# Kernel optimization log

Measured on AMD Instinct MI355X. Metric: run time of the kernel, lower is better.

The kernel has to match this reference:

```python
import jax, jax.numpy as jnp
import numpy as np

N_TAGS = 128
ROOT = 126
END = 127
NEG = -10000.0


def setup_inputs() -> dict:
    key = jax.random.key(0)
    k1, k2, k3, k4 = jax.random.split(key, 4)
    bsz, T = 256, 256
    feats = jax.random.normal(k1, (bsz, T, N_TAGS), jnp.float32)
    tags = jax.random.randint(k2, (bsz, T), 0, ROOT)  # never ROOT/END
    lengths = jax.random.randint(k3, (bsz,), 1, T + 1)
    mask = (jnp.arange(T)[None, :] < lengths[:, None]).astype(jnp.int32)
    # xavier_normal_: std = gain * sqrt(2 / (fan_in + fan_out))
    std = np.float32(np.sqrt(2.0 / (2 * N_TAGS)))
    lt = jax.random.normal(k4, (N_TAGS, N_TAGS), jnp.float32) * std
    lt = lt.at[:, ROOT].set(NEG).at[END, :].set(NEG)
    return {"feats": feats, "tags": tags, "mask": mask, "log_transitions": lt}


def _neg_log_likelihood(feats, log_transitions, tags, maskf):
    bsz, T, n = feats.shape
    # ---- forward belief propagation (log partition) ----
    init = log_transitions[ROOT, :] + feats[:, 0, :]  # [b, n]

    def step(fv, xs):
        feat, m = xs  # feat: [b, n], m: [b]
        # logsumexp over previous tag axis; emission is independent of it
        nxt = jax.nn.logsumexp(fv[:, :, None] + log_transitions[None, :, :], axis=1) + feat
        return jnp.where(m[:, None] > 0, nxt, fv), None

    feats_t = jnp.swapaxes(feats, 0, 1)  # [T, b, n]
    fv, _ = jax.lax.scan(step, init, (feats_t[1:], maskf[:, 1:].T))
    partition = jax.nn.logsumexp(fv + log_transitions[:, END][None, :], axis=1)  # [b]

    # ---- gold path score ----
    trans_tt = log_transitions[tags[:, :-1], tags[:, 1:]]                         # [b, T-1]
    emis = jnp.take_along_axis(feats[:, :-1, :], tags[:, :-1, None], axis=2)[..., 0]
    scores = log_transitions[ROOT, tags[:, 0]]
    scores = scores + jnp.sum(trans_tt * maskf[:, 1:] + emis * maskf[:, :-1], axis=1)
    last_idx = (maskf.sum(axis=1) - 1.0).astype(jnp.int32)                         # [b]
    last_tags = jnp.take_along_axis(tags, last_idx[:, None], axis=1)[:, 0]
    last_input = jnp.take_along_axis(feats[:, -1, :], last_tags[:, None], axis=1)[:, 0]
    scores = scores + log_transitions[last_tags, END] + last_input * maskf[:, -1]

    return jnp.mean(partition - scores)


def reference(feats, tags, mask, log_transitions):
    maskf = mask.astype(feats.dtype)
    return _neg_log_likelihood(feats, log_transitions, tags, maskf)
```

## Files before the change

kernel.cpp:

```cpp
#include <hip/hip_runtime.h>
#include <hip/hip_bf16.h>

#define N_TAGS 128
#define T_LEN  256
#define BSZ    256
#define ROOT_T 126
#define END_T  127

typedef _Float16 h2 __attribute__((ext_vector_type(2)));
typedef int   i32x4 __attribute__((ext_vector_type(4)));

static __device__ __forceinline__ h2 pkrtz(float a, float b) {
  return __builtin_bit_cast(h2, __builtin_amdgcn_cvt_pkrtz(a, b));
}
static __device__ __forceinline__ float rfl(float x) {
  return __int_as_float(__builtin_amdgcn_readfirstlane(__float_as_int(x)));
}
static __device__ __forceinline__ h2 rdl(h2 v, int k) {
  return __builtin_bit_cast(h2, __builtin_amdgcn_readlane(__builtin_bit_cast(int, v), k));
}
static __device__ __forceinline__ float fdot2(h2 a, h2 b, float c) {
#if __has_builtin(__builtin_amdgcn_fdot2)
  return __builtin_amdgcn_fdot2(a, b, c, false);
#else
  float d;
  asm("v_dot2_f32_f16 %0, %1, %2, %3" : "=v"(d) : "v"(a), "v"(b), "v"(c));
  return d;
#endif
}
static __device__ __forceinline__ float wave_max(float x) {
  #pragma unroll
  for (int d = 1; d < 64; d <<= 1) x = fmaxf(x, __shfl_xor(x, d));
  return x;
}

static __device__ __forceinline__ void dotRL(h2 vp,
                                             const h2 (&EA)[64], const h2 (&EB)[64],
                                             float& s0, float& s1) {
  float a0=0.f,a1=0.f,a2=0.f,a3=0.f, b0=0.f,b1=0.f,b2=0.f,b3=0.f;
  #pragma unroll
  for (int q = 0; q < 64; q += 4) {
    const h2 u0 = rdl(vp, q + 0);
    const h2 u1 = rdl(vp, q + 1);
    const h2 u2 = rdl(vp, q + 2);
    const h2 u3 = rdl(vp, q + 3);
    a0 = fdot2(u0, EA[q + 0], a0);  b0 = fdot2(u0, EB[q + 0], b0);
    a1 = fdot2(u1, EA[q + 1], a1);  b1 = fdot2(u1, EB[q + 1], b1);
    a2 = fdot2(u2, EA[q + 2], a2);  b2 = fdot2(u2, EB[q + 2], b2);
    a3 = fdot2(u3, EA[q + 3], a3);  b3 = fdot2(u3, EB[q + 3], b3);
  }
  s0 = (a0 + a1) + (a2 + a3);
  s1 = (b0 + b1) + (b2 + b3);
}

__global__ void
__attribute__((amdgpu_flat_work_group_size(128, 128), amdgpu_waves_per_eu(1, 1)))
crf_fwd_kernel(
    const float* __restrict__ feats,
    const int*   __restrict__ tags,
    const int*   __restrict__ mask,
    const float* __restrict__ lt,
    float*       __restrict__ per_batch)
{
  const int b    = blockIdx.x;
  const int tid  = threadIdx.x;
  const int lane = tid & 63;
  const int wave = tid >> 6;

  __shared__ float stage[32 * 129];
  __shared__ float bb[N_TAGS];
  __shared__ float sred[2];

  const float* fb = feats + (size_t)b * T_LEN * N_TAGS;
  const int*   tb = tags  + b * T_LEN;

  int len;
  {
    const i32x4 mv = ((const i32x4*)(mask + b * T_LEN))[lane];
    int v = mv.x + mv.y + mv.z + mv.w;
    #pragma unroll
    for (int d = 1; d < 64; d <<= 1) v += __shfl_xor(v, d);
    len = __builtin_amdgcn_readfirstlane(v);
  }

  h2 EA[64], EB[64];
  #pragma unroll
  for (int c = 0; c < 4; ++c) {
    __syncthreads();
    #pragma unroll
    for (int rr = 0; rr < 32; ++rr)
      stage[rr * 129 + tid] = __expf(lt[(c * 32 + rr) * N_TAGS + tid]);
    __syncthreads();
    if (wave == 0) {
      #pragma unroll
      for (int k = 0; k < 16; ++k) {
        h2 ea, eb;
        ea.x = (_Float16)stage[(2*k)   * 129 + 2*lane];
        ea.y = (_Float16)stage[(2*k+1) * 129 + 2*lane];
        eb.x = (_Float16)stage[(2*k)   * 129 + 2*lane + 1];
        eb.y = (_Float16)stage[(2*k+1) * 129 + 2*lane + 1];
        EA[c*16 + k] = ea;
        EB[c*16 + k] = eb;
      }
    } else if ((lane >> 4) == c) {
      const int r0 = 2 * lane - 32 * c;
      #pragma unroll
      for (int q = 0; q < 64; ++q) {
        h2 ea, eb;
        ea.x = (_Float16)stage[r0       * 129 + 2*q];
        ea.y = (_Float16)stage[r0       * 129 + 2*q + 1];
        eb.x = (_Float16)stage[(r0 + 1) * 129 + 2*q];
        eb.y = (_Float16)stage[(r0 + 1) * 129 + 2*q + 1];
        EA[q] = ea;
        EB[q] = eb;
      }
    }
  }

  float st0, st1;

  if (wave == 0) {
    {
      const float2 f0 = ((const float2*)fb)[lane];
      st0 = lt[ROOT_T * N_TAGS + 2*lane]     + f0.x;
      st1 = lt[ROOT_T * N_TAGS + 2*lane + 1] + f0.y;
    }
    float2 buf[4];
    buf[1] = ((const float2*)(fb + 1 * N_TAGS))[lane];
    buf[2] = ((const float2*)(fb + 2 * N_TAGS))[lane];
    buf[3] = ((const float2*)(fb + 3 * N_TAGS))[lane];
    buf[0] = ((const float2*)(fb + 4 * N_TAGS))[lane];
    float m_cur = rfl(st0) + 2.0f;
    h2 vp = pkrtz(__expf(st0 - m_cur), __expf(st1 - m_cur));

    #pragma unroll 4
    for (int t = 1; t <= 128; ++t) {
      float s0, s1;
      dotRL(vp, EA, EB, s0, s1);
      const float2 fa = buf[t & 3];
      buf[t & 3] = ((const float2*)(fb + (t + 4) * N_TAGS))[lane];
      const float nf0 = m_cur + __logf(s0) + fa.x;
      const float nf1 = m_cur + __logf(s1) + fa.y;
      const bool act = (t < len);
      st0 = act ? nf0 : st0;  st1 = act ? nf1 : st1;
      const float m = rfl(st0) + 2.0f;
      vp = pkrtz(__expf(st0 - m), __expf(st1 - m));
      m_cur = m;
    }
  } else {
    st0 = lt[(2*lane)     * N_TAGS + END_T];
    st1 = lt[(2*lane + 1) * N_TAGS + END_T];
    const float2 fw = ((const float2*)(fb + 255 * N_TAGS))[lane];
    float2 buf[4];
    buf[0] = ((const float2*)(fb + 254 * N_TAGS))[lane];
    buf[1] = ((const float2*)(fb + 253 * N_TAGS))[lane];
    buf[2] = ((const float2*)(fb + 252 * N_TAGS))[lane];
    buf[3] = ((const float2*)(fb + 251 * N_TAGS))[lane];
    const float y0i = st0 + fw.x, y1i = st1 + fw.y;
    float m_cur = rfl(y0i) + 2.0f;
    h2 vp = pkrtz(__expf(y0i - m_cur), __expf(y1i - m_cur));

    const int kmin = 256 - len;
    #pragma unroll 4
    for (int k = 0; k <= 127; ++k) {
      float s0, s1;
      dotRL(vp, EA, EB, s0, s1);
      const float nb0 = m_cur + __logf(s0);
      const float nb1 = m_cur + __logf(s1);
      const bool act = (k >= kmin) && (k <= 126);
      st0 = act ? nb0 : st0;  st1 = act ? nb1 : st1;
      const float2 fa = buf[k & 3];
      buf[k & 3] = ((const float2*)(fb + (250 - k) * N_TAGS))[lane];
      const float y0 = st0 + fa.x, y1 = st1 + fa.y;
      const float m = rfl(y0) + 2.0f;
      vp = pkrtz(__expf(y0 - m), __expf(y1 - m));
      m_cur = m;
    }
    bb[2*lane]     = st0;
    bb[2*lane + 1] = st1;
  }
  __syncthreads();

  float c = 0.f;
  #pragma unroll
  for (int q = 0; q < 2; ++q) {
    const int t  = tid + q * N_TAGS;
    const int tg = tb[t];
    if (t == 0)                           c += lt[ROOT_T * N_TAGS + tg];
    if (t >= 1 && t < len)                c += lt[tb[t - 1] * N_TAGS + tg];
    if (t < len && t <= T_LEN - 2)        c += fb[t * N_TAGS + tg];
    if (t == len - 1)                     c += lt[tg * N_TAGS + END_T];
    if (t == T_LEN - 1 && len == T_LEN)   c += fb[t * N_TAGS + tg];
  }
  #pragma unroll
  for (int d = 1; d < 64; d <<= 1) c += __shfl_xor(c, d);
  if (lane == 0) sred[wave] = c;

  float part = 0.f;
  if (wave == 0) {
    const float x0 = st0 + bb[2*lane];
    const float x1 = st1 + bb[2*lane + 1];
    const float mw = wave_max(fmaxf(x0, x1));
    float e = __expf(x0 - mw) + __expf(x1 - mw);
    #pragma unroll
    for (int d = 1; d < 64; d <<= 1) e += __shfl_xor(e, d);
    part = mw + __logf(e);
  }
  __syncthreads();

  if (tid == 0) per_batch[b] = part - (sred[0] + sred[1]);
}

__global__ __launch_bounds__(256) void crf_reduce_kernel(
    const float* __restrict__ per_batch, float* __restrict__ out)
{
  const int tid = threadIdx.x;
  float v = per_batch[tid] * (1.0f / BSZ);
  #pragma unroll
  for (int d = 1; d < 64; d <<= 1) v += __shfl_xor(v, d);
  __shared__ float r[4];
  if ((tid & 63) == 0) r[tid >> 6] = v;
  __syncthreads();
  if (tid == 0) out[0] = r[0] + r[1] + r[2] + r[3];
}

extern "C" void kernel_launch(void* const* d_in, const int* in_sizes, int n_in,
                              void* d_out, int out_size, void* d_ws, size_t ws_size,
                              hipStream_t stream) {
  (void)in_sizes; (void)n_in; (void)out_size; (void)ws_size;
  const float* feats = (const float*)d_in[0];
  const int*   tags  = (const int*)d_in[1];
  const int*   mask  = (const int*)d_in[2];
  const float* lt    = (const float*)d_in[3];
  float* per_batch = (float*)d_ws;

  crf_fwd_kernel<<<BSZ, 128, 0, stream>>>(feats, tags, mask, lt, per_batch);
  crf_reduce_kernel<<<1, 256, 0, stream>>>(per_batch, (float*)d_out);
}
```

Baseline: 76.20 us.

## Run CRF recursion in scaled linear domain and broadcast forward vector via LDS

Both recursions now keep their state as scaled probabilities in the linear domain, with a running log-scale. Each step drops the per-element log/exp pair and uses one reciprocal plus one log of a single lane's value. The forward wave also stops broadcasting its state with 64 readlanes and instead double-buffers it through shared memory, reading it back as vectorized h8 loads. This shortens the serial per-step dependency chain, at the cost of fp16 range and precision risk in the scaled state and an LDS write/read round trip on each step.

```diff
diff --git a/kernel.cpp b/kernel.cpp
--- a/kernel.cpp
+++ b/kernel.cpp
@@ -6,8 +6,10 @@
 #define BSZ    256
 #define ROOT_T 126
 #define END_T  127
+#define LOG16  2.7725887222397811f
 
 typedef _Float16 h2 __attribute__((ext_vector_type(2)));
+typedef _Float16 h8 __attribute__((ext_vector_type(8)));
 typedef int   i32x4 __attribute__((ext_vector_type(4)));
 
 static __device__ __forceinline__ h2 pkrtz(float a, float b) {
@@ -32,6 +34,27 @@
   #pragma unroll
   for (int d = 1; d < 64; d <<= 1) x = fmaxf(x, __shfl_xor(x, d));
   return x;
+}
+
+static __device__ __forceinline__ void dot128(const h2* __restrict__ psv,
+                                              const h2 (&EA)[64], const h2 (&EB)[64],
+                                              float& s0, float& s1) {
+  const h8* pv = (const h8*)psv;
+  float a0=0.f,a1=0.f,a2=0.f,a3=0.f, b0=0.f,b1=0.f,b2=0.f,b3=0.f;
+  #pragma unroll
+  for (int r = 0; r < 16; ++r) {
+    const h8 v = pv[r];
+    const h2 p0 = __builtin_shufflevector(v, v, 0, 1);
+    const h2 p1 = __builtin_shufflevector(v, v, 2, 3);
+    const h2 p2 = __builtin_shufflevector(v, v, 4, 5);
+    const h2 p3 = __builtin_shufflevector(v, v, 6, 7);
+    a0 = fdot2(p0, EA[4*r+0], a0);  a1 = fdot2(p1, EA[4*r+1], a1);
+    a2 = fdot2(p2, EA[4*r+2], a2);  a3 = fdot2(p3, EA[4*r+3], a3);
+    b0 = fdot2(p0, EB[4*r+0], b0);  b1 = fdot2(p1, EB[4*r+1], b1);
+    b2 = fdot2(p2, EB[4*r+2], b2);  b3 = fdot2(p3, EB[4*r+3], b3);
+  }
+  s0 = (a0 + a1) + (a2 + a3);
+  s1 = (b0 + b1) + (b2 + b3);
 }
 
 static __device__ __forceinline__ void dotRL(h2 vp,
@@ -67,6 +90,7 @@
   const int lane = tid & 63;
   const int wave = tid >> 6;
 
+  __shared__ __align__(16) h2 psF[2][64];
   __shared__ float stage[32 * 129];
   __shared__ float bb[N_TAGS];
   __shared__ float sred[2];
@@ -117,67 +141,75 @@
     }
   }
 
-  float st0, st1;
+  float xa0 = 0.f, xa1 = 0.f;
 
   if (wave == 0) {
+    float st0, st1;
     {
       const float2 f0 = ((const float2*)fb)[lane];
       st0 = lt[ROOT_T * N_TAGS + 2*lane]     + f0.x;
       st1 = lt[ROOT_T * N_TAGS + 2*lane + 1] + f0.y;
     }
+    float Lf = rfl(st0) + 2.0f;
+    h2 p = pkrtz(__expf(st0 - Lf), __expf(st1 - Lf));
+    psF[1][lane] = p;
     float2 buf[4];
     buf[1] = ((const float2*)(fb + 1 * N_TAGS))[lane];
     buf[2] = ((const float2*)(fb + 2 * N_TAGS))[lane];
     buf[3] = ((const float2*)(fb + 3 * N_TAGS))[lane];
     buf[0] = ((const float2*)(fb + 4 * N_TAGS))[lane];
-    float m_cur = rfl(st0) + 2.0f;
-    h2 vp = pkrtz(__expf(st0 - m_cur), __expf(st1 - m_cur));
 
     #pragma unroll 4
     for (int t = 1; t <= 128; ++t) {
+      const int R = t & 1, W = R ^ 1;
       float s0, s1;
-      dotRL(vp, EA, EB, s0, s1);
-      const float2 fa = buf[t & 3];
+      dot128(psF[R], EA, EB, s0, s1);
+      const float2 f = buf[t & 3];
       buf[t & 3] = ((const float2*)(fb + (t + 4) * N_TAGS))[lane];
-      const float nf0 = m_cur + __logf(s0) + fa.x;
-      const float nf1 = m_cur + __logf(s1) + fa.y;
+      const float ef0 = __expf(f.x), ef1 = __expf(f.y);
+      const float t0 = s0 * ef0, t1 = s1 * ef1;
       const bool act = (t < len);
-      st0 = act ? nf0 : st0;  st1 = act ? nf1 : st1;
-      const float m = rfl(st0) + 2.0f;
-      vp = pkrtz(__expf(st0 - m), __expf(st1 - m));
-      m_cur = m;
-    }
+      const float r0 = rfl(t0);
+      const float kk = __builtin_amdgcn_rcpf(r0) * 0.0625f;
+      const h2 pn = pkrtz(t0 * kk, t1 * kk);
+      p = act ? pn : p;
+      Lf += act ? (__logf(r0) + LOG16) : 0.0f;
+      psF[W][lane] = p;
+    }
+    xa0 = Lf + __logf((float)p.x);
+    xa1 = Lf + __logf((float)p.y);
   } else {
-    st0 = lt[(2*lane)     * N_TAGS + END_T];
-    st1 = lt[(2*lane + 1) * N_TAGS + END_T];
+    float st0 = lt[(2*lane)     * N_TAGS + END_T];
+    float st1 = lt[(2*lane + 1) * N_TAGS + END_T];
+    float Lb = rfl(st0) + 2.0f;
+    h2 u = pkrtz(__expf(st0 - Lb), __expf(st1 - Lb));
     const float2 fw = ((const float2*)(fb + 255 * N_TAGS))[lane];
+    h2 efh = pkrtz(__expf(fw.x), __expf(fw.y));
+    h2 r = u * efh;
     float2 buf[4];
     buf[0] = ((const float2*)(fb + 254 * N_TAGS))[lane];
     buf[1] = ((const float2*)(fb + 253 * N_TAGS))[lane];
     buf[2] = ((const float2*)(fb + 252 * N_TAGS))[lane];
     buf[3] = ((const float2*)(fb + 251 * N_TAGS))[lane];
-    const float y0i = st0 + fw.x, y1i = st1 + fw.y;
-    float m_cur = rfl(y0i) + 2.0f;
-    h2 vp = pkrtz(__expf(y0i - m_cur), __expf(y1i - m_cur));
 
     const int kmin = 256 - len;
     #pragma unroll 4
     for (int k = 0; k <= 127; ++k) {
       float s0, s1;
-      dotRL(vp, EA, EB, s0, s1);
-      const float nb0 = m_cur + __logf(s0);
-      const float nb1 = m_cur + __logf(s1);
+      dotRL(r, EA, EB, s0, s1);
       const bool act = (k >= kmin) && (k <= 126);
-      st0 = act ? nb0 : st0;  st1 = act ? nb1 : st1;
-      const float2 fa = buf[k & 3];
+      const float r0 = rfl(s0);
+      const float kk = __builtin_amdgcn_rcpf(r0) * 0.0625f;
+      const h2 un = pkrtz(s0 * kk, s1 * kk);
+      u = act ? un : u;
+      Lb += act ? (__logf(r0) + LOG16) : 0.0f;
+      const float2 w2 = buf[k & 3];
       buf[k & 3] = ((const float2*)(fb + (250 - k) * N_TAGS))[lane];
-      const float y0 = st0 + fa.x, y1 = st1 + fa.y;
-      const float m = rfl(y0) + 2.0f;
-      vp = pkrtz(__expf(y0 - m), __expf(y1 - m));
-      m_cur = m;
-    }
-    bb[2*lane]     = st0;
-    bb[2*lane + 1] = st1;
+      efh = pkrtz(__expf(w2.x), __expf(w2.y));
+      r = u * efh;
+    }
+    bb[2*lane]     = Lb + __logf((float)u.x);
+    bb[2*lane + 1] = Lb + __logf((float)u.y);
   }
   __syncthreads();
 
@@ -198,8 +230,8 @@
 
   float part = 0.f;
   if (wave == 0) {
-    const float x0 = st0 + bb[2*lane];
-    const float x1 = st1 + bb[2*lane + 1];
+    const float x0 = xa0 + bb[2*lane];
+    const float x1 = xa1 + bb[2*lane + 1];
     const float mw = wave_max(fmaxf(x0, x1));
     float e = __expf(x0 - mw) + __expf(x1 - mw);
     #pragma unroll
```

After: 102.6 us. 1.35x slower.
